# Optimization experiments

Hardware: AMD Instinct MI355X
Metric: run time of the kernel (lower is better)

Reference implementation:

```python
import jax, jax.numpy as jnp
import numpy as np

POOL = 7                     # cfg.POOLING_SIZE
PRE = 2 * POOL               # pre_pool_size (max_pool=True path)
LEVEL_HW = (256, 128, 64, 32)  # square H=W of P2..P5 for a 1024x1024 image


def setup_inputs() -> dict:
    key = jax.random.key(0)
    ks = jax.random.split(key, 8)
    C = 256
    feats = {f"p{i + 2}": jax.random.normal(ks[i], (1, C, s, s), dtype=jnp.float32)
             for i, s in enumerate(LEVEL_HW)}
    N = 1000
    IMG = 1024.0
    x1 = jax.random.uniform(ks[4], (N,), minval=0.0, maxval=IMG - 33.0)
    y1 = jax.random.uniform(ks[5], (N,), minval=0.0, maxval=IMG - 33.0)
    w = jax.random.uniform(ks[6], (N,), minval=32.0, maxval=512.0)
    h = jax.random.uniform(ks[7], (N,), minval=32.0, maxval=512.0)
    x2 = jnp.minimum(x1 + w, IMG - 1.0)
    y2 = jnp.minimum(y1 + h, IMG - 1.0)
    rois = jnp.stack([jnp.zeros((N,), jnp.float32), x1, y1, x2, y2], axis=1)
    inp = dict(feats)
    inp["rois"] = rois
    return inp


def _crop_pool_fpn(p2, p3, p4, p5, rois):
    """Faithful vectorized version of Network._crop_pool_layer_fpn (max_pool=True).

    Per-ROI FPN level select, affine-grid + bilinear grid_sample
    (align_corners=True semantics, zeros padding), then 2x2 max pool.
    """
    levels = (p2, p3, p4, p5)
    C = p2.shape[1]
    Hm = p2.shape[2]  # largest (P2) map; all levels padded up to this
    # Pad every level into one [L, Hm, Wm, C] array (NHWC for clean gathers).
    feats = jnp.stack([
        jnp.pad(jnp.transpose(f[0], (1, 2, 0)),
                ((0, Hm - f.shape[2]), (0, Hm - f.shape[3]), (0, 0)))
        for f in levels])

    x1, y1, x2, y2 = rois[:, 1], rois[:, 2], rois[:, 3], rois[:, 4]
    w = jnp.where(x2 - x1 <= 0, 1e-14, x2 - x1)
    h = jnp.where(y2 - y1 <= 0, 1e-14, y2 - y1)
    kf = 4.0 + jnp.log2(jnp.sqrt(w * h) / 224.0)   # k0 + log2(sqrt(wh)/224)
    kf = jnp.clip(kf, 2.0, 5.0)                     # clamp BEFORE round (as in source)
    k = jnp.round(kf)
    scale = 2.0 ** k
    lvl = k.astype(jnp.int32) - 2                   # [N] in [0,4)
    x1s, y1s, x2s, y2s = x1 / scale, y1 / scale, x2 / scale, y2 / scale

    # affine_grid(theta) + align_corners=True grid_sample collapses to direct
    # pixel coords: px = (x1+x2)/2 + t*(x2-x1)/2, t = linspace(-1, 1, PRE).
    t = jnp.linspace(-1.0, 1.0, PRE)
    px = (x1s + x2s)[:, None] * 0.5 + t[None, :] * ((x2s - x1s)[:, None] * 0.5)  # [N,PRE]
    py = (y1s + y2s)[:, None] * 0.5 + t[None, :] * ((y2s - y1s)[:, None] * 0.5)
    PX = jnp.broadcast_to(px[:, None, :], (px.shape[0], PRE, PRE))  # [N,PRE,PRE]
    PY = jnp.broadcast_to(py[:, :, None], (py.shape[0], PRE, PRE))

    HWl = jnp.asarray(LEVEL_HW, jnp.float32)[lvl][:, None, None]  # per-ROI level size (square)
    x0 = jnp.floor(PX)
    y0 = jnp.floor(PY)
    dx = PX - x0
    dy = PY - y0

    def gather(yi, xi):
        inb = ((xi >= 0) & (xi < HWl) & (yi >= 0) & (yi < HWl)).astype(feats.dtype)
        yc = jnp.clip(yi, 0, Hm - 1).astype(jnp.int32)
        xc = jnp.clip(xi, 0, Hm - 1).astype(jnp.int32)
        v = feats[lvl[:, None, None], yc, xc]      # [N,PRE,PRE,C]
        return v * inb[..., None]                   # zeros padding

    out = (gather(y0, x0) * ((1 - dy) * (1 - dx))[..., None]
           + gather(y0, x0 + 1) * ((1 - dy) * dx)[..., None]
           + gather(y0 + 1, x0) * (dy * (1 - dx))[..., None]
           + gather(y0 + 1, x0 + 1) * (dy * dx)[..., None])  # [N,PRE,PRE,C]

    crops = jnp.transpose(out, (0, 3, 1, 2))        # [N,C,PRE,PRE]
    N = crops.shape[0]
    crops = crops.reshape(N, C, POOL, 2, POOL, 2).max(axis=(3, 5))  # 2x2 max pool
    return crops                                     # [N,C,POOL,POOL]


def reference(p2, p3, p4, p5, rois):
    return _crop_pool_fpn(p2, p3, p4, p5, rois)
```

## Files before the change

### kernel.cpp

```cpp
#include <hip/hip_runtime.h>
#include <math.h>

#define C_CH 256
#define PRE 14
#define NPOOL 7
#define PIX (NPOOL * NPOOL)
#define OUT_PER_ROI (C_CH * PIX)
#define HALF_C 128
#define HALF_OUT (HALF_C * PIX)
#define SROW 132

#define OFF_P2 0
#define OFF_P3 16777216u
#define OFF_P4 20971520u
#define OFF_P5 22020096u
#define WS_ELEMS 22282240u

static __device__ __forceinline__ unsigned short f2bf(float f) {
    unsigned int u = __float_as_uint(f);
    unsigned int r = (u + 0x7FFFu + ((u >> 16) & 1u)) >> 16;
    return (unsigned short)r;
}
static __device__ __forceinline__ float bf2f(unsigned short b) {
    return __uint_as_float(((unsigned int)b) << 16);
}

__global__ __launch_bounds__(256) void transpose_all_k(
    const float* __restrict__ p2, const float* __restrict__ p3,
    const float* __restrict__ p4, const float* __restrict__ p5,
    unsigned short* __restrict__ ws) {
    __shared__ float tile[64][65];
    int b = blockIdx.x;
    const float* __restrict__ src;
    int HW2; unsigned int off;
    if (b < 4096)      { src = p2; HW2 = 65536; off = OFF_P2; }
    else if (b < 5120) { src = p3; HW2 = 16384; off = OFF_P3; b -= 4096; }
    else if (b < 5376) { src = p4; HW2 = 4096;  off = OFF_P4; b -= 5120; }
    else               { src = p5; HW2 = 1024;  off = OFF_P5; b -= 5376; }
    const int c0  = (b & 3) << 6;
    const int hw0 = (b >> 2) << 6;
    const int lane = threadIdx.x & 63;
    const int row  = threadIdx.x >> 6;
    #pragma unroll
    for (int cc = row; cc < 64; cc += 4)
        tile[cc][lane] = src[(size_t)(c0 + cc) * HW2 + hw0 + lane];
    __syncthreads();
    #pragma unroll
    for (int hh = row; hh < 64; hh += 4)
        ws[off + (size_t)(hw0 + hh) * C_CH + c0 + lane] = f2bf(tile[lane][hh]);
}

template <bool HWC>
__global__ __launch_bounds__(256, 6) void roi_align_k(
    const float* __restrict__ p2, const float* __restrict__ p3,
    const float* __restrict__ p4, const float* __restrict__ p5,
    const unsigned short* __restrict__ ws, const float* __restrict__ rois,
    float* __restrict__ out) {

    __shared__ float sxw0[PRE], sxw1[PRE], syw0[PRE], syw1[PRE];
    __shared__ int   sxc0[PRE], sxc1[PRE], syc0[PRE], syc1[PRE];
    __shared__ float sout[PIX * SROW];

    const int n   = blockIdx.x;
    const int ch0 = blockIdx.y << 7;
    const float x1 = rois[n * 5 + 1];
    const float y1 = rois[n * 5 + 2];
    const float x2 = rois[n * 5 + 3];
    const float y2 = rois[n * 5 + 4];

    float w = x2 - x1; w = (w <= 0.f) ? 1e-14f : w;
    float h = y2 - y1; h = (h <= 0.f) ? 1e-14f : h;
    float kf = 4.f + log2f(sqrtf(w * h) * (1.f / 224.f));
    kf = fminf(fmaxf(kf, 2.f), 5.f);
    const float kr = rintf(kf);
    const int   lvl = (int)kr - 2;
    const float scale = exp2f(kr);
    const int   HW = 256 >> lvl;

    const int t = threadIdx.x;

    if (t < 2 * PRE) {
        const bool isx = t < PRE;
        const int  j = isx ? t : t - PRE;
        const float a1 = isx ? x1 : y1;
        const float a2 = isx ? x2 : y2;
        const float a1s = a1 / scale, a2s = a2 / scale;
        const float cen  = (a1s + a2s) * 0.5f;
        const float half = (a2s - a1s) * 0.5f;
        const float tt = -1.f + (2.f / 13.f) * (float)j;
        const float p  = cen + tt * half;
        const float p0 = floorf(p);
        const float d  = p - p0;
        const float HWf = (float)HW;
        const float m0 = (p0 >= 0.f && p0 < HWf) ? 1.f : 0.f;
        const float m1 = (p0 + 1.f >= 0.f && p0 + 1.f < HWf) ? 1.f : 0.f;
        const int c0i = min(max((int)p0, 0), HW - 1);
        const int c1i = min(max((int)p0 + 1, 0), HW - 1);
        if (isx) { sxw0[j] = (1.f - d) * m0; sxw1[j] = d * m1; sxc0[j] = c0i; sxc1[j] = c1i; }
        else     { syw0[j] = (1.f - d) * m0; syw1[j] = d * m1; syc0[j] = c0i; syc1[j] = c1i; }
    }
    __syncthreads();

    const int g     = t & 31;
    const int ph    = t >> 5;
    const int cbase = ch0 + (g << 2);

    const unsigned short* __restrict__ fb = nullptr;
    const float* __restrict__ fbF = nullptr;
    if (HWC) {
        const unsigned int off = (lvl == 0) ? OFF_P2 : (lvl == 1) ? OFF_P3 : (lvl == 2) ? OFF_P4 : OFF_P5;
        fb = ws + off + cbase;
    } else {
        fbF = (lvl == 0) ? p2 : (lvl == 1) ? p3 : (lvl == 2) ? p4 : p5;
    }
    const int HW2 = HW * HW;

    for (int p = ph; p < PIX; p += 8) {
        const int oy = p / 7;
        const int ox = p - oy * 7;
        float4 m = make_float4(-3.4e38f, -3.4e38f, -3.4e38f, -3.4e38f);
        #pragma unroll
        for (int sy = 0; sy < 2; ++sy) {
            const int i = oy * 2 + sy;
            const float wy0 = syw0[i], wy1 = syw1[i];
            const int   yc0 = syc0[i], yc1 = syc1[i];
            #pragma unroll
            for (int sx = 0; sx < 2; ++sx) {
                const int j = ox * 2 + sx;
                const float wx0 = sxw0[j], wx1 = sxw1[j];
                const int   xc0 = sxc0[j], xc1 = sxc1[j];
                float4 v;
                if (HWC) {
                    const ushort4 a00 = *(const ushort4*)(fb + ((yc0 * HW + xc0) << 8));
                    const ushort4 a01 = *(const ushort4*)(fb + ((yc0 * HW + xc1) << 8));
                    const ushort4 a10 = *(const ushort4*)(fb + ((yc1 * HW + xc0) << 8));
                    const ushort4 a11 = *(const ushort4*)(fb + ((yc1 * HW + xc1) << 8));
                    v.x = wy0 * (wx0 * bf2f(a00.x) + wx1 * bf2f(a01.x)) + wy1 * (wx0 * bf2f(a10.x) + wx1 * bf2f(a11.x));
                    v.y = wy0 * (wx0 * bf2f(a00.y) + wx1 * bf2f(a01.y)) + wy1 * (wx0 * bf2f(a10.y) + wx1 * bf2f(a11.y));
                    v.z = wy0 * (wx0 * bf2f(a00.z) + wx1 * bf2f(a01.z)) + wy1 * (wx0 * bf2f(a10.z) + wx1 * bf2f(a11.z));
                    v.w = wy0 * (wx0 * bf2f(a00.w) + wx1 * bf2f(a01.w)) + wy1 * (wx0 * bf2f(a10.w) + wx1 * bf2f(a11.w));
                } else {
                    float vv[4];
                    #pragma unroll
                    for (int k = 0; k < 4; ++k) {
                        const size_t cb = (size_t)(cbase + k) * HW2;
                        const float a00 = fbF[cb + yc0 * HW + xc0];
                        const float a01 = fbF[cb + yc0 * HW + xc1];
                        const float a10 = fbF[cb + yc1 * HW + xc0];
                        const float a11 = fbF[cb + yc1 * HW + xc1];
                        vv[k] = wy0 * (wx0 * a00 + wx1 * a01) + wy1 * (wx0 * a10 + wx1 * a11);
                    }
                    v.x = vv[0]; v.y = vv[1]; v.z = vv[2]; v.w = vv[3];
                }
                m.x = fmaxf(m.x, v.x);
                m.y = fmaxf(m.y, v.y);
                m.z = fmaxf(m.z, v.z);
                m.w = fmaxf(m.w, v.w);
            }
        }
        *(float4*)&sout[p * SROW + (g << 2)] = m;
    }
    __syncthreads();

    const size_t ob = (size_t)n * OUT_PER_ROI + (size_t)ch0 * PIX;
    for (int o = t; o < HALF_OUT; o += 256) {
        const int c  = o / PIX;
        const int pp = o - c * PIX;
        out[ob + o] = sout[pp * SROW + c];
    }
}

extern "C" void kernel_launch(void* const* d_in, const int* in_sizes, int n_in,
                              void* d_out, int out_size, void* d_ws, size_t ws_size,
                              hipStream_t stream) {
    const float* p2   = (const float*)d_in[0];
    const float* p3   = (const float*)d_in[1];
    const float* p4   = (const float*)d_in[2];
    const float* p5   = (const float*)d_in[3];
    const float* rois = (const float*)d_in[4];
    float* out = (float*)d_out;
    const int N = in_sizes[4] / 5;

    const size_t need = (size_t)WS_ELEMS * sizeof(unsigned short);
    if (ws_size >= need) {
        unsigned short* ws = (unsigned short*)d_ws;
        transpose_all_k<<<5440, 256, 0, stream>>>(p2, p3, p4, p5, ws);
        roi_align_k<true><<<dim3(N, 2), 256, 0, stream>>>(p2, p3, p4, p5, ws, rois, out);
    } else {
        roi_align_k<false><<<dim3(N, 2), 256, 0, stream>>>(p2, p3, p4, p5, nullptr, rois, out);
    }
}
```

Baseline: 58.24 us.

## Rewrite NCHW-to-NHWC bf16 transpose with wide vector loads and swizzled LDS tiles

The transpose kernel now has each block handle 128 spatial positions across all 256 channels. Each thread reads float4 from four channels, converts to bf16 in registers, and writes packed ushort4 into an XOR-swizzled LDS tile. It then emits 16-byte coalesced stores of full 512-byte channel rows. This cuts the grid from 5440 to 680 blocks and replaces the scalar 4-byte loads and 2-byte stores, aiming at the memory-bound transpose that precedes ROI align. The cost is 66KB of LDS per block, which lowers occupancy, and fewer, larger blocks.

```diff
diff --git a/kernel.cpp b/kernel.cpp
--- a/kernel.cpp
+++ b/kernel.cpp
@@ -16,6 +16,8 @@
 #define OFF_P5 22020096u
 #define WS_ELEMS 22282240u
 
+#define RB 528
+
 static __device__ __forceinline__ unsigned short f2bf(float f) {
     unsigned int u = __float_as_uint(f);
     unsigned int r = (u + 0x7FFFu + ((u >> 16) & 1u)) >> 16;
@@ -29,25 +31,55 @@
     const float* __restrict__ p2, const float* __restrict__ p3,
     const float* __restrict__ p4, const float* __restrict__ p5,
     unsigned short* __restrict__ ws) {
-    __shared__ float tile[64][65];
+    __shared__ unsigned char lds[128 * RB];
+
     int b = blockIdx.x;
     const float* __restrict__ src;
     int HW2; unsigned int off;
-    if (b < 4096)      { src = p2; HW2 = 65536; off = OFF_P2; }
-    else if (b < 5120) { src = p3; HW2 = 16384; off = OFF_P3; b -= 4096; }
-    else if (b < 5376) { src = p4; HW2 = 4096;  off = OFF_P4; b -= 5120; }
-    else               { src = p5; HW2 = 1024;  off = OFF_P5; b -= 5376; }
-    const int c0  = (b & 3) << 6;
-    const int hw0 = (b >> 2) << 6;
-    const int lane = threadIdx.x & 63;
-    const int row  = threadIdx.x >> 6;
+    if (b < 512)      { src = p2; HW2 = 65536; off = OFF_P2; }
+    else if (b < 640) { src = p3; HW2 = 16384; off = OFF_P3; b -= 512; }
+    else if (b < 672) { src = p4; HW2 = 4096;  off = OFF_P4; b -= 640; }
+    else              { src = p5; HW2 = 1024;  off = OFF_P5; b -= 672; }
+    const int hw0 = b << 7;
+
+    const int t   = threadIdx.x;
+    const int hwq = t & 31;
+    const int cg  = t >> 5;
+
+    const int key = (hwq & 7) << 4;
+
     #pragma unroll
-    for (int cc = row; cc < 64; cc += 4)
-        tile[cc][lane] = src[(size_t)(c0 + cc) * HW2 + hw0 + lane];
+    for (int s = 0; s < 8; ++s) {
+        const int c0 = (cg << 2) + (s << 5);
+        const float* g = src + (size_t)c0 * HW2 + hw0 + (hwq << 2);
+        const float4 a0 = *(const float4*)(g);
+        const float4 a1 = *(const float4*)(g + HW2);
+        const float4 a2 = *(const float4*)(g + 2 * (size_t)HW2);
+        const float4 a3 = *(const float4*)(g + 3 * (size_t)HW2);
+        const int cb = (c0 << 1) ^ key;
+        unsigned char* base = &lds[(hwq << 2) * RB + cb];
+        ushort4 w;
+        w.x = f2bf(a0.x); w.y = f2bf(a1.x); w.z = f2bf(a2.x); w.w = f2bf(a3.x);
+        *(ushort4*)(base) = w;
+        w.x = f2bf(a0.y); w.y = f2bf(a1.y); w.z = f2bf(a2.y); w.w = f2bf(a3.y);
+        *(ushort4*)(base + RB) = w;
+        w.x = f2bf(a0.z); w.y = f2bf(a1.z); w.z = f2bf(a2.z); w.w = f2bf(a3.z);
+        *(ushort4*)(base + 2 * RB) = w;
+        w.x = f2bf(a0.w); w.y = f2bf(a1.w); w.z = f2bf(a2.w); w.w = f2bf(a3.w);
+        *(ushort4*)(base + 3 * RB) = w;
+    }
     __syncthreads();
+
+    char* __restrict__ dstb = (char*)(ws + off + ((size_t)hw0 << 8));
+    const int chunk = t & 31;
+    const int hwl   = t >> 5;
     #pragma unroll
-    for (int hh = row; hh < 64; hh += 4)
-        ws[off + (size_t)(hw0 + hh) * C_CH + c0 + lane] = f2bf(tile[lane][hh]);
+    for (int p = 0; p < 16; ++p) {
+        const int hw = (p << 3) + hwl;
+        const int k2 = ((hw >> 2) & 7) << 4;
+        const uint4 v = *(const uint4*)&lds[hw * RB + ((chunk << 4) ^ k2)];
+        *(uint4*)(dstb + hw * 512 + (chunk << 4)) = v;
+    }
 }
 
 template <bool HWC>
@@ -184,7 +216,7 @@
     const size_t need = (size_t)WS_ELEMS * sizeof(unsigned short);
     if (ws_size >= need) {
         unsigned short* ws = (unsigned short*)d_ws;
-        transpose_all_k<<<5440, 256, 0, stream>>>(p2, p3, p4, p5, ws);
+        transpose_all_k<<<680, 256, 0, stream>>>(p2, p3, p4, p5, ws);
         roi_align_k<true><<<dim3(N, 2), 256, 0, stream>>>(p2, p3, p4, p5, ws, rois, out);
     } else {
         roi_align_k<false><<<dim3(N, 2), 256, 0, stream>>>(p2, p3, p4, p5, nullptr, rois, out);
```

New measurement: 56.25 us. 1.04x faster.
